# Kernel tuning notes

Hardware: AMD Instinct MI355X
Metric: run time of the kernel (lower is better)

Reference implementation:

```python
import jax, jax.numpy as jnp
import numpy as np

HEAD_DIM = 64
SELECT = 256  # number of selected rows/cols (m)
NUM_ITER = 4  # Newton-Schulz iterations


def _select_idx(T, mask, m):
    # top-k over sum of features (select_type='sum'), done under stop_gradient (torch.no_grad)
    somme = jax.lax.stop_gradient(jnp.sum(T, axis=-1))  # [B,H,N]
    neg = -jnp.finfo(somme.dtype).max
    somme = jnp.where(mask[:, None, :], somme, neg)
    _, idx = jax.lax.top_k(somme, m)  # [B,H,m], descending like argsort(descending=True)[:m]
    return idx


def _gather_rows(T, idx):
    # T: [B,H,N,D], idx: [B,H,m] -> [B,H,m,D]  (index_select over flattened (b h n))
    return jnp.take_along_axis(T, idx[..., None], axis=2)


def _iterative_inv(mat, num_iter):
    m = mat.shape[-1]
    I = jnp.eye(m, dtype=mat.dtype)
    K = mat
    # V0 = K^T / max_j(sum_i K_ij)
    scale = 1.0 / jnp.max(jnp.sum(K, axis=-2), axis=-1)[:, :, None, None]
    V = scale * jnp.swapaxes(K, -1, -2)
    for _ in range(num_iter):
        KV = jnp.matmul(K, V)
        V = jnp.matmul(0.25 * V, 13.0 * I - jnp.matmul(KV, 15.0 * I - jnp.matmul(KV, 7.0 * I - KV)))
    return V


def setup_inputs() -> dict:
    key = jax.random.key(0)
    kq, kk, kv = jax.random.split(key, 3)
    B, H, N, D = 2, 8, 4096, HEAD_DIM
    Q = jax.random.normal(kq, (B, H, N, D), dtype=jnp.float32)
    K = jax.random.normal(kk, (B, H, N, D), dtype=jnp.float32)
    V = jax.random.normal(kv, (B, H, N, D), dtype=jnp.float32)
    mask = jnp.ones((B, N), dtype=bool)
    return {"Q": Q, "K": K, "V": V, "mask": mask}


def reference(Q, K, V, mask):
    m = SELECT
    Qs = Q / np.sqrt(HEAD_DIM).astype(np.float32)
    # select_mode='default' -> index_select_different: indices for K from K, for Q from (scaled) Q
    idx_k = _select_idx(K, mask, m)
    idx_q = _select_idx(Qs, mask, m)
    nc = _gather_rows(K, idx_k)   # [B,H,m,D] selected columns (from K)
    nr = _gather_rows(Qs, idx_k := idx_q if False else idx_q) if False else _gather_rows(Qs, idx_q)  # [B,H,m,D]
    c = jnp.einsum('bhnd,bhmd->bhnm', Qs, nc)   # [B,H,N,m]
    r = jnp.einsum('bhmd,bhnd->bhmn', nr, K)    # [B,H,m,N]
    neg = -jnp.finfo(Qs.dtype).max
    r = jnp.where(mask[:, None, None, :], r, neg)
    kernel_1 = jax.nn.softmax(c, axis=-1)                 # [B,H,N,m]
    u = _gather_rows(kernel_1, idx_q)                     # [B,H,m,m]
    kernel_3 = jax.nn.softmax(r, axis=-1)                 # [B,H,m,N]
    kernel_2_inv = _iterative_inv(u, NUM_ITER)            # [B,H,m,m]
    RV = jnp.matmul(kernel_3, V)                          # [B,H,m,D]
    X = jnp.matmul(kernel_1, jnp.matmul(kernel_2_inv, RV))  # [B,H,N,D]
    return X
```

## Files before the change

### kernel.cpp

```cpp
#include <hip/hip_runtime.h>
#include <float.h>


#define G    16
#define NSEQ 4096
#define DH   64
#define MSEL 256
#define NSL  16

typedef __attribute__((ext_vector_type(8))) short short8;
typedef __attribute__((ext_vector_type(4))) float floatx4;
typedef __attribute__((ext_vector_type(4))) unsigned short ushort4v;
typedef unsigned short ush;

static __device__ __forceinline__ ush f2b(float x) {
    union { float f; unsigned u; } c{x};
    unsigned r = c.u + 0x7FFFu + ((c.u >> 16) & 1u);
    return (ush)(r >> 16);
}
static __device__ __forceinline__ float b2f(ush h) {
    union { unsigned u; float f; } c{(unsigned)h << 16};
    return c.f;
}
static __device__ __forceinline__ void split_store(ush* __restrict__ h, ush* __restrict__ l,
                                                   int off, float4 v, float scale) {
    float a0 = v.x * scale, a1 = v.y * scale, a2 = v.z * scale, a3 = v.w * scale;
    ush h0 = f2b(a0), h1 = f2b(a1), h2 = f2b(a2), h3 = f2b(a3);
    ushort4v hv = { h0, h1, h2, h3 };
    ushort4v lv = { f2b(a0 - b2f(h0)), f2b(a1 - b2f(h1)), f2b(a2 - b2f(h2)), f2b(a3 - b2f(h3)) };
    *(ushort4v*)&h[off] = hv;
    *(ushort4v*)&l[off] = lv;
}
static __device__ __forceinline__ floatx4 mfma3(short8 ah, short8 al, short8 bh, short8 bl, floatx4 acc) {
    acc = __builtin_amdgcn_mfma_f32_16x16x32_bf16(al, bh, acc, 0, 0, 0);
    acc = __builtin_amdgcn_mfma_f32_16x16x32_bf16(ah, bl, acc, 0, 0, 0);
    acc = __builtin_amdgcn_mfma_f32_16x16x32_bf16(ah, bh, acc, 0, 0, 0);
    return acc;
}

__global__ __launch_bounds__(256) void rowsum_kernel(const float* __restrict__ Q, const float* __restrict__ K,
                                                     float* __restrict__ sumQ, float* __restrict__ sumK,
                                                     float* __restrict__ k2) {
    long row = (long)blockIdx.x * 16 + (threadIdx.x >> 4);
    int c4 = (threadIdx.x & 15) * 4;
    float4 q = *(const float4*)(Q + row * DH + c4);
    float4 k = *(const float4*)(K + row * DH + c4);
    float qs = q.x + q.y + q.z + q.w;
    float ks = k.x + k.y + k.z + k.w;
    float k2s = k.x * k.x + k.y * k.y + k.z * k.z + k.w * k.w;
#pragma unroll
    for (int off = 8; off; off >>= 1) {
        qs += __shfl_xor(qs, off); ks += __shfl_xor(ks, off); k2s += __shfl_xor(k2s, off);
    }
    if ((threadIdx.x & 15) == 0) { sumQ[row] = qs; sumK[row] = ks; k2[row] = k2s; }
}

__global__ __launch_bounds__(256) void topk_select(const float* __restrict__ sumQ, const float* __restrict__ sumK,
                                                   int* __restrict__ idxQ, int* __restrict__ idxK,
                                                   const float* __restrict__ k2, float* __restrict__ Kmax2) {
    __shared__ unsigned red[4];
    __shared__ float redf[4];
    __shared__ unsigned eqpre[64];
    __shared__ unsigned cnt_sel;
    int g = blockIdx.x, which = blockIdx.y;
    const float* s = (which ? sumK : sumQ) + (long)g * NSEQ;
    int* out = (which ? idxK : idxQ) + g * MSEL;
    int t = threadIdx.x, lane = t & 63, wid = t >> 6;
    unsigned k[16];
#pragma unroll
    for (int i = 0; i < 16; i++) {
        unsigned u = __float_as_uint(s[t + 256 * i]);
        k[i] = (u & 0x80000000u) ? ~u : (u | 0x80000000u);
    }
    unsigned T = 0;
    for (int b = 31; b >= 0; b--) {
        unsigned trial = T | (1u << b);
        int c = 0;
#pragma unroll
        for (int i = 0; i < 16; i++) c += (k[i] >= trial);
#pragma unroll
        for (int off = 32; off; off >>= 1) c += __shfl_xor(c, off);
        __syncthreads();
        if (lane == 0) red[wid] = (unsigned)c;
        __syncthreads();
        unsigned tot = red[0] + red[1] + red[2] + red[3];
        if (tot == MSEL) { T = trial; break; }
        if (tot > MSEL) T = trial;
    }
    int cg = 0;
#pragma unroll
    for (int i = 0; i < 16; i++) cg += (k[i] > T);
#pragma unroll
    for (int off = 32; off; off >>= 1) cg += __shfl_xor(cg, off);
    __syncthreads();
    if (lane == 0) red[wid] = (unsigned)cg;
    if (t == 0) cnt_sel = 0;
    __syncthreads();
    unsigned ngreater = red[0] + red[1] + red[2] + red[3];
    unsigned want_eq = MSEL - ngreater;
#pragma unroll
    for (int i = 0; i < 16; i++) {
        unsigned long long be = __ballot(k[i] == T);
        if (lane == 0) eqpre[i * 4 + wid] = (unsigned)__popcll(be);
    }
    __syncthreads();
    if (t == 0) {
        unsigned run = 0;
        for (int j = 0; j < 64; j++) { unsigned c = eqpre[j]; eqpre[j] = run; run += c; }
    }
    __syncthreads();
#pragma unroll
    for (int i = 0; i < 16; i++) {
        int idx = t + 256 * i;
        unsigned long long lt = (1ull << lane) - 1;
        bool gt = (k[i] > T);
        unsigned long long bg = __ballot(gt);
        unsigned wbase = 0;
        if (lane == 0) wbase = atomicAdd(&cnt_sel, (unsigned)__popcll(bg));
        wbase = __shfl((int)wbase, 0);
        if (gt) out[wbase + __popcll(bg & lt)] = idx;
        bool eq = (k[i] == T);
        unsigned long long be = __ballot(eq);
        if (eq) {
            unsigned rank = eqpre[i * 4 + wid] + (unsigned)__popcll(be & lt);
            if (rank < want_eq) out[ngreater + rank] = idx;
        }
    }
    if (which == 1) {
        float mx = 0.f;
#pragma unroll
        for (int i = 0; i < 16; i++) mx = fmaxf(mx, k2[(long)g * NSEQ + t + 256 * i]);
#pragma unroll
        for (int off = 32; off; off >>= 1) mx = fmaxf(mx, __shfl_xor(mx, off));
        __syncthreads();
        if (lane == 0) redf[wid] = mx;
        __syncthreads();
        if (t == 0) Kmax2[g] = fmaxf(fmaxf(redf[0], redf[1]), fmaxf(redf[2], redf[3]));
    }
}

__global__ __launch_bounds__(256) void gather_kernel(const float* __restrict__ Q, const float* __restrict__ K,
                                                     const int* __restrict__ idxQ, const int* __restrict__ idxK,
                                                     const float* __restrict__ Kmax2,
                                                     float* __restrict__ nr,
                                                     ush* __restrict__ ncH, ush* __restrict__ ncL,
                                                     float* __restrict__ Mb) {
    int wid = threadIdx.x >> 6, lane = threadIdx.x & 63;
    long t = (long)blockIdx.x * 4 + wid;
    long g = t >> 8;
    int iq = idxQ[t], ik = idxK[t];
    float qv = Q[(g * NSEQ + iq) * DH + lane] * 0.125f;
    nr[t * DH + lane] = qv;
    float kv = K[(g * NSEQ + ik) * DH + lane];
    ush h = f2b(kv);
    ncH[t * DH + lane] = h;
    ncL[t * DH + lane] = f2b(kv - b2f(h));
    float n2 = qv * qv;
#pragma unroll
    for (int off = 32; off; off >>= 1) n2 += __shfl_xor(n2, off);
    if (lane == 0) Mb[t] = sqrtf(n2 * Kmax2[g]);
}

__global__ __launch_bounds__(256, 4) void flash_rv(const float* __restrict__ nr, const float* __restrict__ K,
                                                   const float* __restrict__ V, const float* __restrict__ Mb,
                                                   float* __restrict__ Lp, float* __restrict__ RVp) {
    __shared__ __align__(16) ush B1h[64 * 72];
    __shared__ __align__(16) ush B1l[64 * 72];
    __shared__ __align__(16) ush Ph[64 * 72];
    __shared__ float msh[64];
    __shared__ float lred[64][2];
    int ns = blockIdx.x, s = blockIdx.y, g = blockIdx.z;
    int t = threadIdx.x, lane = t & 63, w = t >> 6;
    int wr = w >> 1, wc = w & 1, ml = lane & 15, quad = lane >> 4;
    int lr = t >> 2, lq = t & 3;
    const float* nrg = nr + (long)g * 16384 + (long)s * 64 * 64;
    const float* Kg  = K + (long)g * 262144 + (long)ns * 256 * 64;
    const float* Vg  = V + (long)g * 262144 + (long)ns * 256 * 64;
    short8 Ah[2][2], Al[2][2];
#pragma unroll
    for (int i2 = 0; i2 < 2; i2++)
#pragma unroll
        for (int kq = 0; kq < 2; kq++) {
            const float* p = nrg + (wr * 32 + i2 * 16 + ml) * 64 + kq * 32 + quad * 8;
            float4 f0 = *(const float4*)p;
            float4 f1 = *(const float4*)(p + 4);
            float vals[8] = { f0.x, f0.y, f0.z, f0.w, f1.x, f1.y, f1.z, f1.w };
            short8 hh, ll;
#pragma unroll
            for (int j = 0; j < 8; j++) {
                ush h = f2b(vals[j]);
                hh[j] = (short)h;
                ll[j] = (short)f2b(vals[j] - b2f(h));
            }
            Ah[i2][kq] = hh; Al[i2][kq] = ll;
        }
    if (t < 64) msh[t] = Mb[g * 256 + s * 64 + t];
    float lsum[2][4] = {};
    floatx4 acc[2][2] = {};
    int vn = t >> 2, vdq = (t & 3) * 16;
    for (int it = 0; it < 4; it++) {
        __syncthreads();
        float4 kv[4], vv[4];
#pragma unroll
        for (int q = 0; q < 4; q++) kv[q] = *(const float4*)(Kg + (long)(it * 64 + lr) * 64 + lq * 16 + q * 4);
#pragma unroll
        for (int q = 0; q < 4; q++) vv[q] = *(const float4*)(Vg + (long)(it * 64 + vn) * 64 + vdq + q * 4);
#pragma unroll
        for (int q = 0; q < 4; q++) split_store(B1h, B1l, lr * 72 + lq * 16 + q * 4, kv[q], 1.0f);
        __syncthreads();
        floatx4 sa[2][2] = {};
#pragma unroll
        for (int kq = 0; kq < 2; kq++) {
            short8 b0h = *(const short8*)&B1h[(wc * 32 + ml) * 72 + kq * 32 + quad * 8];
            short8 b0l = *(const short8*)&B1l[(wc * 32 + ml) * 72 + kq * 32 + quad * 8];
            short8 b1h = *(const short8*)&B1h[(wc * 32 + 16 + ml) * 72 + kq * 32 + quad * 8];
            short8 b1l = *(const short8*)&B1l[(wc * 32 + 16 + ml) * 72 + kq * 32 + quad * 8];
            sa[0][0] = mfma3(Ah[0][kq], Al[0][kq], b0h, b0l, sa[0][0]);
            sa[0][1] = mfma3(Ah[0][kq], Al[0][kq], b1h, b1l, sa[0][1]);
            sa[1][0] = mfma3(Ah[1][kq], Al[1][kq], b0h, b0l, sa[1][0]);
            sa[1][1] = mfma3(Ah[1][kq], Al[1][kq], b1h, b1l, sa[1][1]);
        }
        __syncthreads();
#pragma unroll
        for (int i2 = 0; i2 < 2; i2++)
#pragma unroll
            for (int r = 0; r < 4; r++) {
                int row = wr * 32 + i2 * 16 + quad * 4 + r;
                float M = msh[row];
                float p0 = __expf(sa[i2][0][r] - M);
                float p1 = __expf(sa[i2][1][r] - M);
                lsum[i2][r] += p0 + p1;
                Ph[row * 72 + wc * 32 + ml] = f2b(p0);
                Ph[row * 72 + wc * 32 + 16 + ml] = f2b(p1);
            }
#pragma unroll
        for (int q = 0; q < 4; q++)
#pragma unroll
            for (int c = 0; c < 4; c++) {
                int d = vdq + q * 4 + c;
                int addr = d * 72 + ((((vn >> 3) ^ ((d >> 4) & 3)) << 3) | (vn & 7));
                B1h[addr] = f2b((&vv[q].x)[c]);
            }
        __syncthreads();
#pragma unroll
        for (int kq = 0; kq < 2; kq++) {
            short8 a0 = *(const short8*)&Ph[(wr * 32 + ml) * 72 + kq * 32 + quad * 8];
            short8 a1 = *(const short8*)&Ph[(wr * 32 + 16 + ml) * 72 + kq * 32 + quad * 8];
            int nb = kq * 4 + quad;
            short8 b0 = *(const short8*)&B1h[(wc * 32 + ml) * 72 + ((nb ^ (2 * wc)) << 3)];
            short8 b1 = *(const short8*)&B1h[(wc * 32 + 16 + ml) * 72 + ((nb ^ (2 * wc + 1)) << 3)];
            acc[0][0] = __builtin_amdgcn_mfma_f32_16x16x32_bf16(a0, b0, acc[0][0], 0, 0, 0);
            acc[0][1] = __builtin_amdgcn_mfma_f32_16x16x32_bf16(a0, b1, acc[0][1], 0, 0, 0);
            acc[1][0] = __builtin_amdgcn_mfma_f32_16x16x32_bf16(a1, b0, acc[1][0], 0, 0, 0);
            acc[1][1] = __builtin_amdgcn_mfma_f32_16x16x32_bf16(a1, b1, acc[1][1], 0, 0, 0);
        }
    }
#pragma unroll
    for (int i2 = 0; i2 < 2; i2++)
#pragma unroll
        for (int r = 0; r < 4; r++) {
            float v = lsum[i2][r];
#pragma unroll
            for (int off = 8; off; off >>= 1) v += __shfl_xor(v, off);
            if (ml == 0) lred[wr * 32 + i2 * 16 + quad * 4 + r][wc] = v;
        }
    __syncthreads();
    long p = ((long)(g * 4 + s)) * NSL + ns;
    if (t < 64) Lp[p * 64 + t] = lred[t][0] + lred[t][1];
    float* rvp = RVp + p * 4096;
#pragma unroll
    for (int i2 = 0; i2 < 2; i2++)
#pragma unroll
        for (int j2 = 0; j2 < 2; j2++)
#pragma unroll
            for (int r = 0; r < 4; r++)
                rvp[(wr * 32 + i2 * 16 + quad * 4 + r) * 64 + wc * 32 + j2 * 16 + ml] = acc[i2][j2][r];
}

__global__ __launch_bounds__(256) void rv_merge(const float* __restrict__ Lp, const float* __restrict__ RVp,
                                                ush* __restrict__ RVt) {
    int g = blockIdx.y;
    int s = blockIdx.x >> 2, mq = blockIdx.x & 3;
    int t = threadIdx.x;
    int d = t & 63;
    int m0 = mq * 16 + (t >> 6) * 4;
    long pb = ((long)(g * 4 + s)) * NSL;
#pragma unroll
    for (int mm = 0; mm < 4; mm++) {
        int rho = m0 + mm;
        float L = 0.f, val = 0.f;
#pragma unroll
        for (int n = 0; n < NSL; n++) {
            L   += Lp[(pb + n) * 64 + rho];
            val += RVp[(pb + n) * 4096 + rho * 64 + d];
        }
        RVt[(long)g * 16384 + d * 256 + s * 64 + rho] = f2b(val / L);
    }
}

template <int MODE>
__global__ __launch_bounds__(256, 4) void fused_cx(const float* __restrict__ A,
                                                   const ush* __restrict__ ncH, const ush* __restrict__ ncL,
                                                   const ush* __restrict__ WtH, const ush* __restrict__ WtL,
                                                   float* __restrict__ Out, float ascale) {
    __shared__ __align__(16) ush SM[18432];
    ush* Ah = SM;            ush* Al = SM + 4608;
    ush* Bh = SM + 9216;     ush* Bl = SM + 13824;
    ush* Ph = SM;            ush* Pl = SM + 4608;
    ush* Wh = SM + 9216;     ush* Wl = SM + 13824;
    __shared__ float pm[256], ps[256], Mr[64], Lr[64];
    int strip = blockIdx.x, g = blockIdx.y;
    int t = threadIdx.x, lane = t & 63, w = t >> 6;
    int wr = w >> 1, wc = w & 1, ml = lane & 15, quad = lane >> 4;
    int lr = t >> 2, lq = t & 3;
    long aRows = (MODE == 0) ? 4096 : 256;
    const float* Ag = A + (long)g * aRows * 64 + (long)strip * 64 * 64;
    const ush* ncHg = ncH + (long)g * 16384;
    const ush* ncLg = ncL + (long)g * 16384;
#pragma unroll
    for (int q = 0; q < 4; q++) {
        float4 v = *(const float4*)(Ag + lr * 64 + lq * 16 + q * 4);
        split_store(Ah, Al, lr * 72 + lq * 16 + q * 4, v, ascale);
    }
    floatx4 sacc[4][4] = {};
    for (int c = 0; c < 4; c++) {
        __syncthreads();
        {
            const ush* sH = ncHg + (c * 64 + lr) * 64;
            const ush* sL = ncLg + (c * 64 + lr) * 64;
            *(uint4*)&Bh[lr * 72 + lq * 8]       = *(const uint4*)&sH[lq * 8];
            *(uint4*)&Bh[lr * 72 + (lq + 4) * 8] = *(const uint4*)&sH[(lq + 4) * 8];
            *(uint4*)&Bl[lr * 72 + lq * 8]       = *(const uint4*)&sL[lq * 8];
            *(uint4*)&Bl[lr * 72 + (lq + 4) * 8] = *(const uint4*)&sL[(lq + 4) * 8];
        }
        __syncthreads();
#pragma unroll
        for (int kq = 0; kq < 2; kq++) {
            short8 bh = *(const short8*)&Bh[(w * 16 + ml) * 72 + kq * 32 + quad * 8];
            short8 bl = *(const short8*)&Bl[(w * 16 + ml) * 72 + kq * 32 + quad * 8];
#pragma unroll
            for (int i = 0; i < 4; i++) {
                short8 afh = *(const short8*)&Ah[(16 * i + ml) * 72 + kq * 32 + quad * 8];
                short8 afl = *(const short8*)&Al[(16 * i + ml) * 72 + kq * 32 + quad * 8];
                sacc[c][i] = mfma3(afh, afl, bh, bl, sacc[c][i]);
            }
        }
    }
#pragma unroll
    for (int i = 0; i < 4; i++)
#pragma unroll
        for (int r = 0; r < 4; r++) {
            float mx = fmaxf(fmaxf(sacc[0][i][r], sacc[1][i][r]), fmaxf(sacc[2][i][r], sacc[3][i][r]));
#pragma unroll
            for (int off = 8; off; off >>= 1) mx = fmaxf(mx, __shfl_xor(mx, off));
            if (ml == 0) pm[(16 * i + quad * 4 + r) * 4 + w] = mx;
        }
    __syncthreads();
    if (t < 64) Mr[t] = fmaxf(fmaxf(pm[t * 4], pm[t * 4 + 1]), fmaxf(pm[t * 4 + 2], pm[t * 4 + 3]));
    __syncthreads();
#pragma unroll
    for (int i = 0; i < 4; i++)
#pragma unroll
        for (int r = 0; r < 4; r++) {
            int row = 16 * i + quad * 4 + r;
            float M = Mr[row];
            float sum = 0.f;
#pragma unroll
            for (int c = 0; c < 4; c++) {
                float p = __expf(sacc[c][i][r] - M);
                sacc[c][i][r] = p;
                sum += p;
            }
#pragma unroll
            for (int off = 8; off; off >>= 1) sum += __shfl_xor(sum, off);
            if (ml == 0) ps[row * 4 + w] = sum;
        }
    __syncthreads();
    if (t < 64) Lr[t] = ps[t * 4] + ps[t * 4 + 1] + ps[t * 4 + 2] + ps[t * 4 + 3];
    __syncthreads();
    if (MODE == 1) {
        float* ug = Out + (long)g * 65536 + (long)strip * 64 * 256;
#pragma unroll
        for (int i = 0; i < 4; i++)
#pragma unroll
            for (int r = 0; r < 4; r++) {
                int row = 16 * i + quad * 4 + r;
                float inv = 1.0f / Lr[row];
#pragma unroll
                for (int c = 0; c < 4; c++)
                    ug[(long)row * 256 + c * 64 + w * 16 + ml] = sacc[c][i][r] * inv;
            }
        return;
    }
    floatx4 xacc[2][2] = {};
    const ush* wHg = WtH + (long)g * 16384;
    const ush* wLg = WtL + (long)g * 16384;
#pragma unroll
    for (int h = 0; h < 4; h++) {
        __syncthreads();
#pragma unroll
        for (int i = 0; i < 4; i++)
#pragma unroll
            for (int r = 0; r < 4; r++) {
                int row = 16 * i + quad * 4 + r;
                float p = sacc[h][i][r];
                ush hh = f2b(p);
                Ph[row * 72 + w * 16 + ml] = hh;
                Pl[row * 72 + w * 16 + ml] = f2b(p - b2f(hh));
            }
        {
            const ush* sH = wHg + lr * 256 + h * 64;
            const ush* sL = wLg + lr * 256 + h * 64;
            *(uint4*)&Wh[lr * 72 + lq * 8]       = *(const uint4*)&sH[lq * 8];
            *(uint4*)&Wh[lr * 72 + (lq + 4) * 8] = *(const uint4*)&sH[(lq + 4) * 8];
            *(uint4*)&Wl[lr * 72 + lq * 8]       = *(const uint4*)&sL[lq * 8];
            *(uint4*)&Wl[lr * 72 + (lq + 4) * 8] = *(const uint4*)&sL[(lq + 4) * 8];
        }
        __syncthreads();
#pragma unroll
        for (int kq = 0; kq < 2; kq++) {
            short8 a0h = *(const short8*)&Ph[(wr * 32 + ml) * 72 + kq * 32 + quad * 8];
            short8 a0l = *(const short8*)&Pl[(wr * 32 + ml) * 72 + kq * 32 + quad * 8];
            short8 a1h = *(const short8*)&Ph[(wr * 32 + 16 + ml) * 72 + kq * 32 + quad * 8];
            short8 a1l = *(const short8*)&Pl[(wr * 32 + 16 + ml) * 72 + kq * 32 + quad * 8];
            short8 b0h = *(const short8*)&Wh[(wc * 32 + ml) * 72 + kq * 32 + quad * 8];
            short8 b0l = *(const short8*)&Wl[(wc * 32 + ml) * 72 + kq * 32 + quad * 8];
            short8 b1h = *(const short8*)&Wh[(wc * 32 + 16 + ml) * 72 + kq * 32 + quad * 8];
            short8 b1l = *(const short8*)&Wl[(wc * 32 + 16 + ml) * 72 + kq * 32 + quad * 8];
            xacc[0][0] = mfma3(a0h, a0l, b0h, b0l, xacc[0][0]);
            xacc[0][1] = mfma3(a0h, a0l, b1h, b1l, xacc[0][1]);
            xacc[1][0] = mfma3(a1h, a1l, b0h, b0l, xacc[1][0]);
            xacc[1][1] = mfma3(a1h, a1l, b1h, b1l, xacc[1][1]);
        }
    }
    float* outg = Out + (long)g * 262144 + (long)strip * 64 * 64;
#pragma unroll
    for (int i2 = 0; i2 < 2; i2++)
#pragma unroll
        for (int j2 = 0; j2 < 2; j2++)
#pragma unroll
            for (int r = 0; r < 4; r++) {
                int row = wr * 32 + i2 * 16 + quad * 4 + r;
                outg[(long)row * 64 + wc * 32 + j2 * 16 + ml] = xacc[i2][j2][r] / Lr[row];
            }
}

__global__ __launch_bounds__(256) void ns_scale_kernel(const float* __restrict__ u, float* __restrict__ scale) {
    __shared__ float red[4];
    int g = blockIdx.x;
    const float* ug = u + (long)g * MSEL * MSEL;
    int j = threadIdx.x;
    float s = 0.f;
    for (int i = 0; i < MSEL; i++) s += ug[(long)i * MSEL + j];
    int lane = j & 63, wid = j >> 6;
#pragma unroll
    for (int off = 32; off; off >>= 1) s = fmaxf(s, __shfl_xor(s, off));
    if (lane == 0) red[wid] = s;
    __syncthreads();
    if (j == 0) scale[g] = 1.0f / fmaxf(fmaxf(red[0], red[1]), fmaxf(red[2], red[3]));
}

__global__ __launch_bounds__(256) void ns_prep_kernel(const float* __restrict__ u, const float* __restrict__ scale,
                                                      ush* __restrict__ u_bf,
                                                      ush* __restrict__ V0,
                                                      ush* __restrict__ V0t) {
    __shared__ float tile[64][65];
    int g = blockIdx.z, tr = blockIdx.y, tc = blockIdx.x;
    float sc = scale[g];
    long base = (long)g * MSEL * MSEL;
    const float* ug = u + base;
    int cq = (threadIdx.x & 15) * 4, r0 = threadIdx.x >> 4;
#pragma unroll
    for (int i = 0; i < 4; i++) {
        int r = r0 + 16 * i;
        float4 v = *(const float4*)&ug[(long)(tr * 64 + r) * MSEL + tc * 64 + cq];
        long o = base + (long)(tr * 64 + r) * MSEL + tc * 64 + cq;
        ushort4v ub = { f2b(v.x), f2b(v.y), f2b(v.z), f2b(v.w) };
        ushort4v vt = { f2b(sc * v.x), f2b(sc * v.y), f2b(sc * v.z), f2b(sc * v.w) };
        *(ushort4v*)&u_bf[o] = ub;
        *(ushort4v*)&V0t[o]  = vt;
        tile[r][cq] = v.x; tile[r][cq + 1] = v.y; tile[r][cq + 2] = v.z; tile[r][cq + 3] = v.w;
    }
    __syncthreads();
#pragma unroll
    for (int i = 0; i < 4; i++) {
        int r = r0 + 16 * i;
        ushort4v o = { f2b(sc * tile[cq][r]), f2b(sc * tile[cq + 1][r]),
                       f2b(sc * tile[cq + 2][r]), f2b(sc * tile[cq + 3][r]) };
        *(ushort4v*)&V0[base + (long)(tc * 64 + r) * MSEL + tr * 64 + cq] = o;
    }
}

template <int MODE>
__global__ __launch_bounds__(256) void ns_gemm(const ush* __restrict__ A,
                                               const ush* __restrict__ Bt,
                                               ush* __restrict__ OutRM,
                                               ush* __restrict__ OutT,
                                               const ush* __restrict__ KVt_in) {
    const int LD = 40;
    __shared__ __align__(16) ush As[2][64 * LD];
    __shared__ __align__(16) ush Bs[2][64 * LD];
    int g = blockIdx.z, tm = blockIdx.y, tn = blockIdx.x;
    long base = (long)g * 65536;
    const ush* Ag = A + base + (long)tm * 64 * 256;
    const ush* Bg = (MODE == 4) ? Bt + (long)g * 16384 + (long)tn * 64 * 256
                                : Bt + base + (long)tn * 64 * 256;
    int t = threadIdx.x;
    int lr = t >> 2, lq = t & 3;
    int w = t >> 6, lane = t & 63;
    int wr = w >> 1, wc = w & 1;
    int ml = lane & 15, quad = lane >> 4;
    floatx4 acc[2][2] = {};

    uint4 ra = *(const uint4*)(Ag + lr * 256 + lq * 8);
    uint4 rb = *(const uint4*)(Bg + lr * 256 + lq * 8);
    *(uint4*)&As[0][lr * LD + lq * 8] = ra;
    *(uint4*)&Bs[0][lr * LD + lq * 8] = rb;
    ra = *(const uint4*)(Ag + lr * 256 + 32 + lq * 8);
    rb = *(const uint4*)(Bg + lr * 256 + 32 + lq * 8);
    __syncthreads();
#pragma unroll
    for (int c = 0; c < 8; c++) {
        int cb = c & 1, nb = cb ^ 1;
        if (c < 7) {
            *(uint4*)&As[nb][lr * LD + lq * 8] = ra;
            *(uint4*)&Bs[nb][lr * LD + lq * 8] = rb;
        }
        if (c < 6) {
            ra = *(const uint4*)(Ag + lr * 256 + (c + 2) * 32 + lq * 8);
            rb = *(const uint4*)(Bg + lr * 256 + (c + 2) * 32 + lq * 8);
        }
        short8 af0 = *(const short8*)&As[cb][(wr * 32 + ml) * LD + quad * 8];
        short8 af1 = *(const short8*)&As[cb][(wr * 32 + 16 + ml) * LD + quad * 8];
        short8 bf0 = *(const short8*)&Bs[cb][(wc * 32 + ml) * LD + quad * 8];
        short8 bf1 = *(const short8*)&Bs[cb][(wc * 32 + 16 + ml) * LD + quad * 8];
        acc[0][0] = __builtin_amdgcn_mfma_f32_16x16x32_bf16(af0, bf0, acc[0][0], 0, 0, 0);
        acc[0][1] = __builtin_amdgcn_mfma_f32_16x16x32_bf16(af0, bf1, acc[0][1], 0, 0, 0);
        acc[1][0] = __builtin_amdgcn_mfma_f32_16x16x32_bf16(af1, bf0, acc[1][0], 0, 0, 0);
        acc[1][1] = __builtin_amdgcn_mfma_f32_16x16x32_bf16(af1, bf1, acc[1][1], 0, 0, 0);
        __syncthreads();
    }

    int rowb = tm * 64 + wr * 32, colb = tn * 64 + wc * 32;
#pragma unroll
    for (int i = 0; i < 2; i++) {
#pragma unroll
        for (int j = 0; j < 2; j++) {
            int col = colb + j * 16 + ml;
            int r0 = rowb + i * 16 + quad * 4;
            float v[4];
#pragma unroll
            for (int r = 0; r < 4; r++) v[r] = acc[i][j][r];
            if (MODE == 1) {
                ushort4v kv = *(const ushort4v*)&KVt_in[base + (long)col * 256 + r0];
#pragma unroll
                for (int r = 0; r < 4; r++) {
                    v[r] -= 7.0f * b2f(kv[r]);
                    if (r0 + r == col) v[r] += 15.0f;
                }
            } else if (MODE == 2) {
#pragma unroll
                for (int r = 0; r < 4; r++) v[r] = ((r0 + r == col) ? 13.0f : 0.0f) - v[r];
            } else if (MODE == 3) {
#pragma unroll
                for (int r = 0; r < 4; r++) v[r] *= 0.25f;
            }
            if (MODE == 4) {
                ushort4v hv, lv;
#pragma unroll
                for (int r = 0; r < 4; r++) {
                    ush h = f2b(v[r]);
                    hv[r] = h;
                    lv[r] = f2b(v[r] - b2f(h));
                }
                *(ushort4v*)&OutRM[(long)g * 16384 + (long)col * 256 + r0] = hv;
                *(ushort4v*)&OutT[(long)g * 16384 + (long)col * 256 + r0] = lv;
            } else {
                ush h[4];
#pragma unroll
                for (int r = 0; r < 4; r++) h[r] = f2b(v[r]);
                if (MODE == 0 || MODE == 3) {
#pragma unroll
                    for (int r = 0; r < 4; r++) OutRM[base + (long)(r0 + r) * 256 + col] = h[r];
                }
                ushort4v ht = { h[0], h[1], h[2], h[3] };
                *(ushort4v*)&OutT[base + (long)col * 256 + r0] = ht;
            }
        }
    }
}

extern "C" void kernel_launch(void* const* d_in, const int* in_sizes, int n_in,
                              void* d_out, int out_size, void* d_ws, size_t ws_size,
                              hipStream_t stream) {
    (void)in_sizes; (void)n_in; (void)out_size; (void)ws_size;
    const float* Q = (const float*)d_in[0];
    const float* K = (const float*)d_in[1];
    const float* V = (const float*)d_in[2];

    float* ws    = (float*)d_ws;
    float* sumQ  = ws;
    float* sumK  = sumQ + 65536;
    float* k2    = sumK + 65536;
    float* nr    = k2 + 65536;
    float* u     = nr + 262144;
    float* Mb    = u + 1048576;
    float* Kmax2 = Mb + 4096;
    float* scale = Kmax2 + 16;
    float* Lp    = scale + 16 + 32;
    float* RVp   = Lp + 65536;
    int* idxQ    = (int*)(RVp + 4194304);
    int* idxK    = idxQ + 4096;
    ush* ncH     = (ush*)(idxK + 4096);
    ush* ncL     = ncH + 262144;
    ush* WtH     = ncL + 262144;
    ush* WtL     = WtH + 262144;
    ush* RVt     = WtL + 262144;
    ush* u_bf    = RVt + 262144;
    ush* KVb     = u_bf + 1048576;
    ush* KVt     = KVb  + 1048576;
    ush* T2t     = KVt  + 1048576;
    ush* T3t     = T2t  + 1048576;
    ush* Va      = T3t  + 1048576;
    ush* Vat     = Va   + 1048576;
    ush* Vb      = Vat  + 1048576;
    ush* Vbt     = Vb   + 1048576;

    dim3 blk(256);

    hipLaunchKernelGGL(rowsum_kernel, dim3(G * NSEQ / 16), blk, 0, stream, Q, K, sumQ, sumK, k2);
    hipLaunchKernelGGL(topk_select, dim3(G, 2), blk, 0, stream, sumQ, sumK, idxQ, idxK, k2, Kmax2);
    hipLaunchKernelGGL(gather_kernel, dim3(G * MSEL / 4), blk, 0, stream, Q, K, idxQ, idxK, Kmax2, nr, ncH, ncL, Mb);

    hipLaunchKernelGGL(flash_rv, dim3(NSL, 4, G), blk, 0, stream, nr, K, V, Mb, Lp, RVp);
    hipLaunchKernelGGL(rv_merge, dim3(16, G), blk, 0, stream, Lp, RVp, RVt);

    hipLaunchKernelGGL((fused_cx<1>), dim3(4, G), blk, 0, stream, nr, ncH, ncL, (const ush*)0, (const ush*)0, u, 1.0f);

    hipLaunchKernelGGL(ns_scale_kernel, dim3(G), blk, 0, stream, u, scale);
    hipLaunchKernelGGL(ns_prep_kernel, dim3(4, 4, G), blk, 0, stream, u, scale, u_bf, Va, Vat);

    ush* Vc = Va;  ush* Vct = Vat;
    ush* Vn = Vb;  ush* Vnt = Vbt;
    dim3 nsgrid(4, 4, G);
    for (int it = 0; it < 4; it++) {
        hipLaunchKernelGGL((ns_gemm<0>), nsgrid, blk, 0, stream, u_bf, Vct, KVb, KVt, (const ush*)0);
        hipLaunchKernelGGL((ns_gemm<1>), nsgrid, blk, 0, stream, KVb, KVt, (ush*)0, T2t, KVt);
        hipLaunchKernelGGL((ns_gemm<2>), nsgrid, blk, 0, stream, KVb, T2t, (ush*)0, T3t, (const ush*)0);
        hipLaunchKernelGGL((ns_gemm<3>), nsgrid, blk, 0, stream, Vc, T3t, Vn, Vnt, (const ush*)0);
        ush* tp;
        tp = Vc; Vc = Vn; Vn = tp;
        tp = Vct; Vct = Vnt; Vnt = tp;
    }

    hipLaunchKernelGGL((ns_gemm<4>), dim3(1, 4, G), blk, 0, stream, Vc, RVt, WtH, WtL, (const ush*)0);

    hipLaunchKernelGGL((fused_cx<0>), dim3(64, G), blk, 0, stream, Q, ncH, ncL, WtH, WtL, (float*)d_out, 0.125f);
}
```

Measured before the change: 283.1 us.

## Reformulate Newton-Schulz iteration around E=KV, fuse column-sum scale into softmax kernel

Restructures the iterative inverse to track E = K·V directly. Each iteration computes S=E², a fused polynomial P=0.25(13I-15E+7S-E·S), and then batches the E and V updates (E←E·P, V←V·P) into one launch with a doubled grid. The final V·RV product is applied as P·RV followed by V·(P·RV). The column sums needed for the initial scale are accumulated with atomics inside the softmax kernel, which removes the separate scale kernel and folds the scale into the first GEMM. The NS GEMM now stages 128-wide K chunks in a single buffer instead of double-buffered 32-wide chunks. The aim is fewer launches and GEMM passes per iteration, at the cost of more workspace and different bf16 rounding behaviour across the iterations.

```diff
diff --git a/kernel.cpp b/kernel.cpp
--- a/kernel.cpp
+++ b/kernel.cpp
@@ -57,7 +57,8 @@
 
 __global__ __launch_bounds__(256) void topk_select(const float* __restrict__ sumQ, const float* __restrict__ sumK,
                                                    int* __restrict__ idxQ, int* __restrict__ idxK,
-                                                   const float* __restrict__ k2, float* __restrict__ Kmax2) {
+                                                   const float* __restrict__ k2, float* __restrict__ Kmax2,
+                                                   float* __restrict__ colsum) {
     __shared__ unsigned red[4];
     __shared__ float redf[4];
     __shared__ unsigned eqpre[64];
@@ -66,6 +67,7 @@
     const float* s = (which ? sumK : sumQ) + (long)g * NSEQ;
     int* out = (which ? idxK : idxQ) + g * MSEL;
     int t = threadIdx.x, lane = t & 63, wid = t >> 6;
+    if (which == 0) colsum[g * 256 + t] = 0.f;
     unsigned k[16];
 #pragma unroll
     for (int i = 0; i < 16; i++) {
@@ -302,7 +304,8 @@
 __global__ __launch_bounds__(256, 4) void fused_cx(const float* __restrict__ A,
                                                    const ush* __restrict__ ncH, const ush* __restrict__ ncL,
                                                    const ush* __restrict__ WtH, const ush* __restrict__ WtL,
-                                                   float* __restrict__ Out, float ascale) {
+                                                   float* __restrict__ Out, float* __restrict__ colsum,
+                                                   float ascale) {
     __shared__ __align__(16) ush SM[18432];
     ush* Ah = SM;            ush* Al = SM + 4608;
     ush* Bh = SM + 9216;     ush* Bl = SM + 13824;
@@ -379,17 +382,32 @@
     if (t < 64) Lr[t] = ps[t * 4] + ps[t * 4 + 1] + ps[t * 4 + 2] + ps[t * 4 + 3];
     __syncthreads();
     if (MODE == 1) {
+        float invL[4][4];
+#pragma unroll
+        for (int i = 0; i < 4; i++)
+#pragma unroll
+            for (int r = 0; r < 4; r++) invL[i][r] = 1.0f / Lr[16 * i + quad * 4 + r];
         float* ug = Out + (long)g * 65536 + (long)strip * 64 * 256;
 #pragma unroll
         for (int i = 0; i < 4; i++)
 #pragma unroll
             for (int r = 0; r < 4; r++) {
                 int row = 16 * i + quad * 4 + r;
-                float inv = 1.0f / Lr[row];
 #pragma unroll
                 for (int c = 0; c < 4; c++)
-                    ug[(long)row * 256 + c * 64 + w * 16 + ml] = sacc[c][i][r] * inv;
-            }
+                    ug[(long)row * 256 + c * 64 + w * 16 + ml] = sacc[c][i][r] * invL[i][r];
+            }
+#pragma unroll
+        for (int c = 0; c < 4; c++) {
+            float v = 0.f;
+#pragma unroll
+            for (int i = 0; i < 4; i++)
+#pragma unroll
+                for (int r = 0; r < 4; r++) v += sacc[c][i][r] * invL[i][r];
+            v += __shfl_xor(v, 16);
+            v += __shfl_xor(v, 32);
+            if (quad == 0) atomicAdd(&colsum[g * 256 + c * 64 + w * 16 + ml], v);
+        }
         return;
     }
     floatx4 xacc[2][2] = {};
@@ -445,41 +463,31 @@
             }
 }
 
-__global__ __launch_bounds__(256) void ns_scale_kernel(const float* __restrict__ u, float* __restrict__ scale) {
-    __shared__ float red[4];
-    int g = blockIdx.x;
-    const float* ug = u + (long)g * MSEL * MSEL;
-    int j = threadIdx.x;
-    float s = 0.f;
-    for (int i = 0; i < MSEL; i++) s += ug[(long)i * MSEL + j];
-    int lane = j & 63, wid = j >> 6;
-#pragma unroll
-    for (int off = 32; off; off >>= 1) s = fmaxf(s, __shfl_xor(s, off));
-    if (lane == 0) red[wid] = s;
-    __syncthreads();
-    if (j == 0) scale[g] = 1.0f / fmaxf(fmaxf(red[0], red[1]), fmaxf(red[2], red[3]));
-}
-
-__global__ __launch_bounds__(256) void ns_prep_kernel(const float* __restrict__ u, const float* __restrict__ scale,
-                                                      ush* __restrict__ u_bf,
-                                                      ush* __restrict__ V0,
-                                                      ush* __restrict__ V0t) {
+__global__ __launch_bounds__(256) void ns_prep_kernel(const float* __restrict__ u, const float* __restrict__ colsum,
+                                                      ush* __restrict__ u_bf, ush* __restrict__ V0,
+                                                      float* __restrict__ scale) {
     __shared__ float tile[64][65];
+    __shared__ float smax[4];
     int g = blockIdx.z, tr = blockIdx.y, tc = blockIdx.x;
-    float sc = scale[g];
+    int t = threadIdx.x, lane = t & 63, wid = t >> 6;
+    float v = colsum[g * 256 + t];
+#pragma unroll
+    for (int off = 32; off; off >>= 1) v = fmaxf(v, __shfl_xor(v, off));
+    if (lane == 0) smax[wid] = v;
+    __syncthreads();
+    float sc = 1.0f / fmaxf(fmaxf(smax[0], smax[1]), fmaxf(smax[2], smax[3]));
+    if (t == 0 && tr == 0 && tc == 0) scale[g] = sc;
     long base = (long)g * MSEL * MSEL;
     const float* ug = u + base;
-    int cq = (threadIdx.x & 15) * 4, r0 = threadIdx.x >> 4;
+    int cq = (t & 15) * 4, r0 = t >> 4;
 #pragma unroll
     for (int i = 0; i < 4; i++) {
         int r = r0 + 16 * i;
-        float4 v = *(const float4*)&ug[(long)(tr * 64 + r) * MSEL + tc * 64 + cq];
+        float4 vv = *(const float4*)&ug[(long)(tr * 64 + r) * MSEL + tc * 64 + cq];
         long o = base + (long)(tr * 64 + r) * MSEL + tc * 64 + cq;
-        ushort4v ub = { f2b(v.x), f2b(v.y), f2b(v.z), f2b(v.w) };
-        ushort4v vt = { f2b(sc * v.x), f2b(sc * v.y), f2b(sc * v.z), f2b(sc * v.w) };
+        ushort4v ub = { f2b(vv.x), f2b(vv.y), f2b(vv.z), f2b(vv.w) };
         *(ushort4v*)&u_bf[o] = ub;
-        *(ushort4v*)&V0t[o]  = vt;
-        tile[r][cq] = v.x; tile[r][cq + 1] = v.y; tile[r][cq + 2] = v.z; tile[r][cq + 3] = v.w;
+        tile[r][cq] = vv.x; tile[r][cq + 1] = vv.y; tile[r][cq + 2] = vv.z; tile[r][cq + 3] = vv.w;
     }
     __syncthreads();
 #pragma unroll
@@ -492,55 +500,54 @@
 }
 
 template <int MODE>
-__global__ __launch_bounds__(256) void ns_gemm(const ush* __restrict__ A,
-                                               const ush* __restrict__ Bt,
-                                               ush* __restrict__ OutRM,
-                                               ush* __restrict__ OutT,
-                                               const ush* __restrict__ KVt_in) {
-    const int LD = 40;
-    __shared__ __align__(16) ush As[2][64 * LD];
-    __shared__ __align__(16) ush Bs[2][64 * LD];
-    int g = blockIdx.z, tm = blockIdx.y, tn = blockIdx.x;
+__global__ __launch_bounds__(256) void ns2(const ush* __restrict__ A0, const ush* __restrict__ A1,
+                                           const ush* __restrict__ Bt,
+                                           ush* __restrict__ O0rm, ush* __restrict__ O0t,
+                                           ush* __restrict__ O1rm, ush* __restrict__ O1t,
+                                           const ush* __restrict__ Et_in, const ush* __restrict__ St_in,
+                                           const float* __restrict__ scale) {
+    const int LD = 136;
+    __shared__ __align__(16) ush As[64 * LD];
+    __shared__ __align__(16) ush Bs[64 * LD];
+    int z = blockIdx.z, g = z & 15, which = z >> 4;
+    int tm = blockIdx.y, tn = blockIdx.x;
     long base = (long)g * 65536;
+    const ush* A = which ? A1 : A0;
+    ush* Orm = which ? O1rm : O0rm;
+    ush* Ot  = which ? O1t  : O0t;
     const ush* Ag = A + base + (long)tm * 64 * 256;
-    const ush* Bg = (MODE == 4) ? Bt + (long)g * 16384 + (long)tn * 64 * 256
-                                : Bt + base + (long)tn * 64 * 256;
+    long bbase = (MODE >= 3) ? (long)g * 16384 : base;
+    const ush* Bg = Bt + bbase + (long)tn * 64 * 256;
     int t = threadIdx.x;
     int lr = t >> 2, lq = t & 3;
     int w = t >> 6, lane = t & 63;
     int wr = w >> 1, wc = w & 1;
     int ml = lane & 15, quad = lane >> 4;
     floatx4 acc[2][2] = {};
-
-    uint4 ra = *(const uint4*)(Ag + lr * 256 + lq * 8);
-    uint4 rb = *(const uint4*)(Bg + lr * 256 + lq * 8);
-    *(uint4*)&As[0][lr * LD + lq * 8] = ra;
-    *(uint4*)&Bs[0][lr * LD + lq * 8] = rb;
-    ra = *(const uint4*)(Ag + lr * 256 + 32 + lq * 8);
-    rb = *(const uint4*)(Bg + lr * 256 + 32 + lq * 8);
-    __syncthreads();
-#pragma unroll
-    for (int c = 0; c < 8; c++) {
-        int cb = c & 1, nb = cb ^ 1;
-        if (c < 7) {
-            *(uint4*)&As[nb][lr * LD + lq * 8] = ra;
-            *(uint4*)&Bs[nb][lr * LD + lq * 8] = rb;
-        }
-        if (c < 6) {
-            ra = *(const uint4*)(Ag + lr * 256 + (c + 2) * 32 + lq * 8);
-            rb = *(const uint4*)(Bg + lr * 256 + (c + 2) * 32 + lq * 8);
-        }
-        short8 af0 = *(const short8*)&As[cb][(wr * 32 + ml) * LD + quad * 8];
-        short8 af1 = *(const short8*)&As[cb][(wr * 32 + 16 + ml) * LD + quad * 8];
-        short8 bf0 = *(const short8*)&Bs[cb][(wc * 32 + ml) * LD + quad * 8];
-        short8 bf1 = *(const short8*)&Bs[cb][(wc * 32 + 16 + ml) * LD + quad * 8];
-        acc[0][0] = __builtin_amdgcn_mfma_f32_16x16x32_bf16(af0, bf0, acc[0][0], 0, 0, 0);
-        acc[0][1] = __builtin_amdgcn_mfma_f32_16x16x32_bf16(af0, bf1, acc[0][1], 0, 0, 0);
-        acc[1][0] = __builtin_amdgcn_mfma_f32_16x16x32_bf16(af1, bf0, acc[1][0], 0, 0, 0);
-        acc[1][1] = __builtin_amdgcn_mfma_f32_16x16x32_bf16(af1, bf1, acc[1][1], 0, 0, 0);
-        __syncthreads();
-    }
-
+#pragma unroll
+    for (int h = 0; h < 2; h++) {
+        __syncthreads();
+#pragma unroll
+        for (int rr = 0; rr < 4; rr++) {
+            int col = (lq + 4 * rr) * 8;
+            *(uint4*)&As[lr * LD + col] = *(const uint4*)(Ag + lr * 256 + h * 128 + col);
+            *(uint4*)&Bs[lr * LD + col] = *(const uint4*)(Bg + lr * 256 + h * 128 + col);
+        }
+        __syncthreads();
+#pragma unroll
+        for (int kq = 0; kq < 4; kq++) {
+            int ko = kq * 32 + quad * 8;
+            short8 a0 = *(const short8*)&As[(wr * 32 + ml) * LD + ko];
+            short8 a1 = *(const short8*)&As[(wr * 32 + 16 + ml) * LD + ko];
+            short8 b0 = *(const short8*)&Bs[(wc * 32 + ml) * LD + ko];
+            short8 b1 = *(const short8*)&Bs[(wc * 32 + 16 + ml) * LD + ko];
+            acc[0][0] = __builtin_amdgcn_mfma_f32_16x16x32_bf16(a0, b0, acc[0][0], 0, 0, 0);
+            acc[0][1] = __builtin_amdgcn_mfma_f32_16x16x32_bf16(a0, b1, acc[0][1], 0, 0, 0);
+            acc[1][0] = __builtin_amdgcn_mfma_f32_16x16x32_bf16(a1, b0, acc[1][0], 0, 0, 0);
+            acc[1][1] = __builtin_amdgcn_mfma_f32_16x16x32_bf16(a1, b1, acc[1][1], 0, 0, 0);
+        }
+    }
+    float sc = (MODE == 1) ? scale[g] : 1.0f;
     int rowb = tm * 64 + wr * 32, colb = tn * 64 + wc * 32;
 #pragma unroll
     for (int i = 0; i < 2; i++) {
@@ -552,20 +559,20 @@
 #pragma unroll
             for (int r = 0; r < 4; r++) v[r] = acc[i][j][r];
             if (MODE == 1) {
-                ushort4v kv = *(const ushort4v*)&KVt_in[base + (long)col * 256 + r0];
-#pragma unroll
-                for (int r = 0; r < 4; r++) {
-                    v[r] -= 7.0f * b2f(kv[r]);
-                    if (r0 + r == col) v[r] += 15.0f;
-                }
+#pragma unroll
+                for (int r = 0; r < 4; r++) v[r] *= sc;
             } else if (MODE == 2) {
-#pragma unroll
-                for (int r = 0; r < 4; r++) v[r] = ((r0 + r == col) ? 13.0f : 0.0f) - v[r];
-            } else if (MODE == 3) {
-#pragma unroll
-                for (int r = 0; r < 4; r++) v[r] *= 0.25f;
-            }
-            if (MODE == 4) {
+                ushort4v et = *(const ushort4v*)&Et_in[base + (long)col * 256 + r0];
+                ushort4v st = *(const ushort4v*)&St_in[base + (long)col * 256 + r0];
+#pragma unroll
+                for (int r = 0; r < 4; r++)
+                    v[r] = 0.25f * (((r0 + r == col) ? 13.0f : 0.0f)
+                                    - 15.0f * b2f(et[r]) + 7.0f * b2f(st[r]) - v[r]);
+            }
+            if (MODE == 3) {
+                ushort4v ht = { f2b(v[0]), f2b(v[1]), f2b(v[2]), f2b(v[3]) };
+                *(ushort4v*)&Ot[(long)g * 16384 + (long)col * 256 + r0] = ht;
+            } else if (MODE == 4) {
                 ushort4v hv, lv;
 #pragma unroll
                 for (int r = 0; r < 4; r++) {
@@ -573,18 +580,16 @@
                     hv[r] = h;
                     lv[r] = f2b(v[r] - b2f(h));
                 }
-                *(ushort4v*)&OutRM[(long)g * 16384 + (long)col * 256 + r0] = hv;
-                *(ushort4v*)&OutT[(long)g * 16384 + (long)col * 256 + r0] = lv;
+                *(ushort4v*)&O0rm[(long)g * 16384 + (long)col * 256 + r0] = hv;
+                *(ushort4v*)&O0t[(long)g * 16384 + (long)col * 256 + r0] = lv;
             } else {
                 ush h[4];
 #pragma unroll
                 for (int r = 0; r < 4; r++) h[r] = f2b(v[r]);
-                if (MODE == 0 || MODE == 3) {
-#pragma unroll
-                    for (int r = 0; r < 4; r++) OutRM[base + (long)(r0 + r) * 256 + col] = h[r];
-                }
+#pragma unroll
+                for (int r = 0; r < 4; r++) Orm[base + (long)(r0 + r) * 256 + col] = h[r];
                 ushort4v ht = { h[0], h[1], h[2], h[3] };
-                *(ushort4v*)&OutT[base + (long)col * 256 + r0] = ht;
+                *(ushort4v*)&Ot[base + (long)col * 256 + r0] = ht;
             }
         }
     }
@@ -607,7 +612,8 @@
     float* Mb    = u + 1048576;
     float* Kmax2 = Mb + 4096;
     float* scale = Kmax2 + 16;
-    float* Lp    = scale + 16 + 32;
+    float* colsum= scale + 16 + 32;
+    float* Lp    = colsum + 4096;
     float* RVp   = Lp + 65536;
     int* idxQ    = (int*)(RVp + 4194304);
     int* idxK    = idxQ + 4096;
@@ -616,44 +622,65 @@
     ush* WtH     = ncL + 262144;
     ush* WtL     = WtH + 262144;
     ush* RVt     = WtL + 262144;
-    ush* u_bf    = RVt + 262144;
-    ush* KVb     = u_bf + 1048576;
-    ush* KVt     = KVb  + 1048576;
-    ush* T2t     = KVt  + 1048576;
-    ush* T3t     = T2t  + 1048576;
-    ush* Va      = T3t  + 1048576;
-    ush* Vat     = Va   + 1048576;
-    ush* Vb      = Vat  + 1048576;
-    ush* Vbt     = Vb   + 1048576;
+    ush* PRt     = RVt + 262144;
+    ush* u_bf    = PRt + 262144;
+    ush* Vacc_a  = u_bf + 1048576;
+    ush* Vacc_b  = Vacc_a + 1048576;
+    ush* VaccTj  = Vacc_b + 1048576;
+    ush* E_a     = VaccTj + 1048576;
+    ush* Et_a    = E_a + 1048576;
+    ush* E_b     = Et_a + 1048576;
+    ush* Et_b    = E_b + 1048576;
+    ush* Sbuf    = Et_b + 1048576;
+    ush* St      = Sbuf + 1048576;
+    ush* Pbuf    = St + 1048576;
+    ush* Pt      = Pbuf + 1048576;
 
     dim3 blk(256);
 
     hipLaunchKernelGGL(rowsum_kernel, dim3(G * NSEQ / 16), blk, 0, stream, Q, K, sumQ, sumK, k2);
-    hipLaunchKernelGGL(topk_select, dim3(G, 2), blk, 0, stream, sumQ, sumK, idxQ, idxK, k2, Kmax2);
+    hipLaunchKernelGGL(topk_select, dim3(G, 2), blk, 0, stream, sumQ, sumK, idxQ, idxK, k2, Kmax2, colsum);
     hipLaunchKernelGGL(gather_kernel, dim3(G * MSEL / 4), blk, 0, stream, Q, K, idxQ, idxK, Kmax2, nr, ncH, ncL, Mb);
 
     hipLaunchKernelGGL(flash_rv, dim3(NSL, 4, G), blk, 0, stream, nr, K, V, Mb, Lp, RVp);
     hipLaunchKernelGGL(rv_merge, dim3(16, G), blk, 0, stream, Lp, RVp, RVt);
 
-    hipLaunchKernelGGL((fused_cx<1>), dim3(4, G), blk, 0, stream, nr, ncH, ncL, (const ush*)0, (const ush*)0, u, 1.0f);
-
-    hipLaunchKernelGGL(ns_scale_kernel, dim3(G), blk, 0, stream, u, scale);
-    hipLaunchKernelGGL(ns_prep_kernel, dim3(4, 4, G), blk, 0, stream, u, scale, u_bf, Va, Vat);
-
-    ush* Vc = Va;  ush* Vct = Vat;
-    ush* Vn = Vb;  ush* Vnt = Vbt;
-    dim3 nsgrid(4, 4, G);
-    for (int it = 0; it < 4; it++) {
-        hipLaunchKernelGGL((ns_gemm<0>), nsgrid, blk, 0, stream, u_bf, Vct, KVb, KVt, (const ush*)0);
-        hipLaunchKernelGGL((ns_gemm<1>), nsgrid, blk, 0, stream, KVb, KVt, (ush*)0, T2t, KVt);
-        hipLaunchKernelGGL((ns_gemm<2>), nsgrid, blk, 0, stream, KVb, T2t, (ush*)0, T3t, (const ush*)0);
-        hipLaunchKernelGGL((ns_gemm<3>), nsgrid, blk, 0, stream, Vc, T3t, Vn, Vnt, (const ush*)0);
-        ush* tp;
-        tp = Vc; Vc = Vn; Vn = tp;
-        tp = Vct; Vct = Vnt; Vnt = tp;
-    }
-
-    hipLaunchKernelGGL((ns_gemm<4>), dim3(1, 4, G), blk, 0, stream, Vc, RVt, WtH, WtL, (const ush*)0);
-
-    hipLaunchKernelGGL((fused_cx<0>), dim3(64, G), blk, 0, stream, Q, ncH, ncL, WtH, WtL, (float*)d_out, 0.125f);
-}
+    hipLaunchKernelGGL((fused_cx<1>), dim3(4, G), blk, 0, stream, nr, ncH, ncL,
+                       (const ush*)0, (const ush*)0, u, colsum, 1.0f);
+
+    hipLaunchKernelGGL(ns_prep_kernel, dim3(4, 4, G), blk, 0, stream, u, colsum, u_bf, Vacc_a, scale);
+
+    hipLaunchKernelGGL((ns2<1>), dim3(4, 4, G), blk, 0, stream,
+                       u_bf, (const ush*)0, u_bf, E_a, Et_a, (ush*)0, (ush*)0,
+                       (const ush*)0, (const ush*)0, scale);
+
+    ush* E = E_a;  ush* Et = Et_a;
+    ush* En = E_b; ush* Ent = Et_b;
+    ush* Vc = Vacc_a; ush* Vn = Vacc_b;
+    for (int i = 0; i < 4; i++) {
+        hipLaunchKernelGGL((ns2<0>), dim3(4, 4, G), blk, 0, stream,
+                           E, (const ush*)0, Et, Sbuf, St, (ush*)0, (ush*)0,
+                           (const ush*)0, (const ush*)0, (const float*)0);
+        hipLaunchKernelGGL((ns2<2>), dim3(4, 4, G), blk, 0, stream,
+                           Sbuf, (const ush*)0, Et, Pbuf, Pt, (ush*)0, (ush*)0,
+                           Et, St, (const float*)0);
+        if (i < 3) {
+            hipLaunchKernelGGL((ns2<0>), dim3(4, 4, 2 * G), blk, 0, stream,
+                               E, Vc, Pt, En, Ent, Vn, VaccTj,
+                               (const ush*)0, (const ush*)0, (const float*)0);
+            ush* tp;
+            tp = E; E = En; En = tp;
+            tp = Et; Et = Ent; Ent = tp;
+            tp = Vc; Vc = Vn; Vn = tp;
+        }
+    }
+    hipLaunchKernelGGL((ns2<3>), dim3(1, 4, G), blk, 0, stream,
+                       Pbuf, (const ush*)0, RVt, (ush*)0, PRt, (ush*)0, (ush*)0,
+                       (const ush*)0, (const ush*)0, (const float*)0);
+    hipLaunchKernelGGL((ns2<4>), dim3(1, 4, G), blk, 0, stream,
+                       Vc, (const ush*)0, PRt, WtH, WtL, (ush*)0, (ush*)0,
+                       (const ush*)0, (const ush*)0, (const float*)0);
+
+    hipLaunchKernelGGL((fused_cx<0>), dim3(64, G), blk, 0, stream, Q, ncH, ncL, WtH, WtL,
+                       (float*)d_out, (float*)0, 0.125f);
+}
```

After: 262.4 us. -7.3%, faster.
